# Kernel tuning notes

Measured on AMD Instinct MI355X. Metric: run time of the kernel, lower is better.

The kernel has to match this reference:

```python
import jax, jax.numpy as jnp
import numpy as np

N = 8192
K = 64
EPS = 1e-7
BN_EPS = 1e-5


def _norm(x):
    return jnp.sqrt(jnp.sum(x * x, axis=-1, keepdims=True))


def _bn(x, gamma, beta):
    # BatchNorm2d in training mode (batch statistics, biased variance)
    mu = jnp.mean(x, axis=(0, 2, 3), keepdims=True)
    var = jnp.mean((x - mu) ** 2, axis=(0, 2, 3), keepdims=True)
    return gamma.reshape(1, -1, 1, 1) * (x - mu) / jnp.sqrt(var + BN_EPS) + beta.reshape(1, -1, 1, 1)


def _conv1x1(x, w, b):
    # 1x1 conv == per-pixel linear: x [B,C,H,W], w [O,C]
    return jnp.einsum('bchw,oc->bohw', x, w) + b.reshape(1, -1, 1, 1)


def setup_inputs() -> dict:
    key = jax.random.key(0)
    ks = jax.random.split(key, 24)
    d = {}
    d['points'] = jax.random.normal(ks[0], (1, N, 3), jnp.float32)
    # graph_conv weights (torch code re-draws these every forward; here fixed params)
    lim0 = float(np.sqrt(6.0 / (4 + 64)))
    d['gw0'] = jax.random.uniform(ks[1], (4, 64), jnp.float32, -lim0, lim0)
    lim = float(np.sqrt(6.0 / (64 + 64)))
    for i in range(1, 5):
        d[f'gw{i}'] = jax.random.uniform(ks[1 + i], (64, 64), jnp.float32, -lim, lim)
    # mlp_1: 4->64->128, mlp_2: 192->256->1024 (1x1 convs + BN)
    d['c1w'] = jax.random.normal(ks[6], (64, 4), jnp.float32) * 0.1
    d['c1b'] = jnp.zeros((64,), jnp.float32)
    d['bn1g'] = jnp.ones((64,), jnp.float32)
    d['bn1b'] = jnp.zeros((64,), jnp.float32)
    d['c2w'] = jax.random.normal(ks[7], (128, 64), jnp.float32) * 0.1
    d['c2b'] = jnp.zeros((128,), jnp.float32)
    d['bn2g'] = jnp.ones((128,), jnp.float32)
    d['bn2b'] = jnp.zeros((128,), jnp.float32)
    d['c3w'] = jax.random.normal(ks[8], (256, 192), jnp.float32) * 0.05
    d['c3b'] = jnp.zeros((256,), jnp.float32)
    d['bn3g'] = jnp.ones((256,), jnp.float32)
    d['bn3b'] = jnp.zeros((256,), jnp.float32)
    d['c4w'] = jax.random.normal(ks[9], (1024, 256), jnp.float32) * 0.05
    d['c4b'] = jnp.zeros((1024,), jnp.float32)
    d['bn4g'] = jnp.ones((1024,), jnp.float32)
    d['bn4b'] = jnp.zeros((1024,), jnp.float32)
    return d


def _knn_search(points, k):
    # pairwise squared distances via ||a||^2 - 2ab + ||b||^2
    r = jnp.sum(points * points, axis=-1, keepdims=True)          # [1,N,1]
    dis = r - 2.0 * jnp.einsum('bnd,bmd->bnm', points, points) + jnp.swapaxes(r, 1, 2)
    _, idx = jax.lax.top_k(-dis, k)                                # [1,N,K]
    knn_pts = jax.vmap(lambda p, i: p[i])(points, idx)             # [1,N,K,3]
    return knn_pts


def _proj_knn(knn_pts):
    b, n, k, _ = knn_pts.shape
    pc = knn_pts - knn_pts[:, :, :1, :]                            # center on first neighbor (self)
    vn = jnp.sqrt(jnp.sum(pc * pc, axis=-1))                       # [1,N,K]
    id1 = jnp.argmax(vn, axis=-1)                                  # farthest neighbor
    a1 = jnp.take_along_axis(pc, jnp.broadcast_to(id1[:, :, None, None], (b, n, 1, 3)), axis=2)[:, :, 0, :]
    a1 = a1 / (_norm(a1) + EPS)
    a2 = jnp.mean(pc, axis=2)
    a2 = a2 / (_norm(a2) + EPS)
    a3 = a1 + 1.5 * a2
    a3 = a3 / (_norm(a3) + EPS)
    den = _norm(pc) + EPS                                          # [1,N,K,1]
    f1 = jnp.sum(pc * a1[:, :, None, :], axis=-1, keepdims=True) / den
    f2 = jnp.sum(pc * a2[:, :, None, :], axis=-1, keepdims=True) / den
    f3 = jnp.sum(pc * a3[:, :, None, :], axis=-1, keepdims=True) / den
    return jnp.concatenate([f1, f2, f3, vn[..., None]], axis=-1)   # [1,N,K,4]


def _proj_points(points):
    b, n, _ = points.shape
    vn = jnp.sqrt(jnp.sum(points * points, axis=-1))               # [1,N]
    i1 = jnp.argmax(vn, axis=-1)
    i2 = jnp.argmin(vn, axis=-1)
    a1 = jnp.take_along_axis(points, jnp.broadcast_to(i1[:, None, None], (b, 1, 3)), axis=1)[:, 0, :]
    a1 = a1 / (_norm(a1) + EPS)
    a2 = jnp.take_along_axis(points, jnp.broadcast_to(i2[:, None, None], (b, 1, 3)), axis=1)[:, 0, :]
    a2 = a2 / (_norm(a2) + EPS)
    a3 = a1 + 1.5 * a2
    a3 = a3 / (_norm(a3) + EPS)
    den = _norm(points) + EPS                                      # [1,N,1]
    f1 = jnp.sum(points * a1[:, None, :], axis=-1, keepdims=True) / den
    f2 = jnp.sum(points * a2[:, None, :], axis=-1, keepdims=True) / den
    f3 = jnp.sum(points * a3[:, None, :], axis=-1, keepdims=True) / den
    return jnp.concatenate([f1, f2, f3, vn[..., None]], axis=-1)   # [1,N,4]


def reference(points, gw0, gw1, gw2, gw3, gw4,
              c1w, c1b, bn1g, bn1b, c2w, c2b, bn2g, bn2b,
              c3w, c3b, bn3g, bn3b, c4w, c4b, bn4g, bn4b):
    n = points.shape[1]
    # upper branch: KNN -> rotation-invariant local feats -> 5-layer MLP -> max over K
    knn_pts = _knn_search(points, K)
    feat_up = _proj_knn(knn_pts)                                   # [1,N,K,4]
    x = feat_up.reshape(-1, 4)
    for w in (gw0, gw1, gw2, gw3, gw4):
        x = jax.nn.relu(x @ w)
    x = x.reshape(1, n, K, 64)
    emb_up = jnp.max(x, axis=2, keepdims=True)                     # [1,N,1,64]
    emb_up = emb_up.reshape(1, 64, n, 1)                           # raw view (reshape), as in torch
    # lower branch: global rotation-invariant feats -> mlp_1
    feat_down = _proj_points(points)                               # [1,N,4]
    emb_down = feat_down.reshape(1, 4, n, 1)                       # raw view (reshape), as in torch
    h = jax.nn.relu(_bn(_conv1x1(emb_down, c1w, c1b), bn1g, bn1b))
    h = jax.nn.relu(_bn(_conv1x1(h, c2w, c2b), bn2g, bn2b))        # [1,128,N,1]
    emb = jnp.concatenate([emb_up, h], axis=1)                     # [1,192,N,1]
    out = jax.nn.relu(_bn(_conv1x1(emb, c3w, c3b), bn3g, bn3b))
    out = jax.nn.relu(_bn(_conv1x1(out, c4w, c4b), bn4g, bn4b))    # [1,1024,N,1]
    return out
```

## Files before the change

### kernel.cpp

```cpp
#include <hip/hip_runtime.h>
#include <hip/hip_bf16.h>

#define NPTS 8192
#define KNN 64
#define EPSF 1e-7f

#define OFF_P4      0
#define OFF_STATS   32768
#define OFF_PART    36012
#define OFF_FEATDN  36864
#define OFF_WT1     69632
#define OFF_GWT     69888
#define OFF_BW2     79104
#define OFF_BW3     83200
#define OFF_BW4     107776
#define OFF_XB3V    238848
#define OFF_Y1      2336000
#define OFF_Y2      2860288
#define OFF_Y3      3908864
#define OFF_FEATUP  6006016

typedef __bf16 bf16x8 __attribute__((ext_vector_type(8)));
typedef float  f32x4  __attribute__((ext_vector_type(4)));

__device__ __forceinline__ unsigned f2u(float f) {
    unsigned u = __float_as_uint(f);
    return ((int)u >= 0) ? (u | 0x80000000u) : ~u;
}
__device__ __forceinline__ float key_to_f(unsigned long long k) {
    unsigned v = (unsigned)(k >> 32);
    unsigned ob = (v & 0x80000000u) ? (v ^ 0x80000000u) : ~v;
    return __uint_as_float(ob);
}
__device__ __forceinline__ unsigned short f2bf(float x) {
    union { __bf16 h; unsigned short s; } u;
    u.h = (__bf16)x;
    return u.s;
}
__device__ __forceinline__ unsigned packbf2(float lo, float hi) {
    return (unsigned)f2bf(lo) | ((unsigned)f2bf(hi) << 16);
}
__device__ __forceinline__ unsigned long long u64min(unsigned long long a, unsigned long long b){ return a < b ? a : b; }
__device__ __forceinline__ unsigned long long u64max(unsigned long long a, unsigned long long b){ return a < b ? b : a; }

__device__ __forceinline__ unsigned long long sort_merge(
    unsigned long long key, unsigned long long cur, int lane)
{
    #pragma unroll
    for (int k = 2; k <= 64; k <<= 1) {
        #pragma unroll
        for (int j = k >> 1; j > 0; j >>= 1) {
            unsigned long long o = __shfl_xor(key, j);
            bool up = ((lane & k) == 0);
            bool lower = ((lane & j) == 0);
            key = (lower == up) ? u64min(key, o) : u64max(key, o);
        }
    }
    unsigned long long rev = __shfl(key, 63 - lane);
    unsigned long long m = u64min(cur, rev);
    #pragma unroll
    for (int j = 32; j > 0; j >>= 1) {
        unsigned long long o = __shfl_xor(m, j);
        m = ((lane & j) == 0) ? u64min(m, o) : u64max(m, o);
    }
    return m;
}

__global__ __launch_bounds__(256) void prepwt_kernel(
    const float* __restrict__ points,
    const float* __restrict__ c1w, const float* __restrict__ c2w,
    const float* __restrict__ c3w, const float* __restrict__ c4w,
    const float* __restrict__ gw0, const float* __restrict__ gw1,
    const float* __restrict__ gw2, const float* __restrict__ gw3,
    const float* __restrict__ gw4,
    float* __restrict__ ws)
{
    const int t = blockIdx.x * 256 + threadIdx.x;
    const int T = 256 * 256;
    for (int m = t; m < 2944; m += T) ws[OFF_STATS + m] = 0.f;
    for (int m = t; m < 64*4; m += T) { int o = m >> 2, c = m & 3; ws[OFF_WT1 + c*64 + o] = c1w[m]; }

    unsigned short* bw2 = (unsigned short*)(ws + OFF_BW2);
    for (int m = t; m < 128*64; m += T)   bw2[m] = f2bf(c2w[m]);
    unsigned short* bw3 = (unsigned short*)(ws + OFF_BW3);
    for (int m = t; m < 256*192; m += T)  bw3[m] = f2bf(c3w[m]);
    unsigned short* bw4 = (unsigned short*)(ws + OFF_BW4);
    for (int m = t; m < 1024*256; m += T) bw4[m] = f2bf(c4w[m]);

    unsigned short* gwt = (unsigned short*)(ws + OFF_GWT);
    for (int m = t; m < 2048; m += T) {
        int o = m >> 5, i = m & 31;
        gwt[m] = (i < 4) ? f2bf(gw0[i*64 + o]) : (unsigned short)0;
    }
    const float* gsrc[4] = {gw1, gw2, gw3, gw4};
    for (int l = 0; l < 4; ++l) {
        const float* g = gsrc[l];
        unsigned short* dst = gwt + 2048 + l*4096;
        for (int m = t; m < 4096; m += T) { int o = m >> 6, i = m & 63; dst[m] = f2bf(g[i*64 + o]); }
    }

    if (blockIdx.x < 32) {
        const int n = blockIdx.x * 256 + threadIdx.x;
        float x = points[3*n+0], y = points[3*n+1], z = points[3*n+2];
        float rr = x*x + y*y + z*z;
        ((float4*)(ws + OFF_P4))[n] = make_float4(x, y, z, rr);
        float vn = sqrtf(rr);
        unsigned b = __float_as_uint(vn);
        unsigned long long mxk = ((unsigned long long)b << 32) | (unsigned long long)(0xFFFFFFFFu - (unsigned)n);
        unsigned long long mnk = ((unsigned long long)b << 32) | (unsigned long long)(unsigned)n;
        for (int j = 32; j > 0; j >>= 1) {
            mxk = u64max(mxk, __shfl_xor(mxk, j));
            mnk = u64min(mnk, __shfl_xor(mnk, j));
        }
        __shared__ unsigned long long smx[4], smn[4];
        int wid = threadIdx.x >> 6;
        if ((threadIdx.x & 63) == 0) { smx[wid] = mxk; smn[wid] = mnk; }
        __syncthreads();
        if (threadIdx.x == 0) {
            unsigned long long MX = 0ull, MN = ~0ull;
            for (int i = 0; i < 4; ++i) { MX = u64max(MX, smx[i]); MN = u64min(MN, smn[i]); }
            unsigned long long* parts = (unsigned long long*)(ws + OFF_PART);
            parts[2*blockIdx.x + 0] = MX;
            parts[2*blockIdx.x + 1] = MN;
        }
    }
}

__global__ __launch_bounds__(512) void knn_feat_kernel(
    const float4* __restrict__ p4, float4* __restrict__ feat_up,
    float* __restrict__ ws)
{
    __shared__ __align__(16) float4 scand[2048];
    __shared__ unsigned long long queue[8][128];
    const int lane = threadIdx.x & 63;
    const int wid  = threadIdx.x >> 6;
    const int q = blockIdx.x * 8 + wid;

    const float4 qa = p4[q];
    unsigned long long cur = ~0ull;
    float ke = __builtin_inff();
    int qc = 0;
    unsigned long long* Q = queue[wid];

    for (int base = 0; base < NPTS; base += 2048) {
        __syncthreads();
        for (int t = threadIdx.x; t < 2048; t += 512) scand[t] = p4[base + t];
        __syncthreads();
        #pragma unroll 2
        for (int sub = 0; sub < 2048; sub += 128) {
            float4 cd0 = scand[sub + lane];
            float4 cd1 = scand[sub + 64 + lane];
            float dot0 = fmaf(qa.x, cd0.x, fmaf(qa.y, cd0.y, qa.z * cd0.z));
            float dot1 = fmaf(qa.x, cd1.x, fmaf(qa.y, cd1.y, qa.z * cd1.z));
            float e0 = fmaf(-2.f, dot0, cd0.w);
            float e1 = fmaf(-2.f, dot1, cd1.w);
            bool p0 = e0 < ke;
            bool p1 = e1 < ke;
            unsigned long long m0 = __ballot(p0);
            unsigned long long m1 = __ballot(p1);
            if (m0) {
                int prefix = __builtin_amdgcn_mbcnt_hi((unsigned)(m0 >> 32),
                              __builtin_amdgcn_mbcnt_lo((unsigned)m0, 0));
                if (p0) Q[qc + prefix] = ((unsigned long long)f2u(e0) << 32)
                                       | (unsigned long long)(unsigned)(base + sub + lane);
                qc += __popcll(m0);
                if (qc >= 64) {
                    qc -= 64;
                    cur = sort_merge(Q[qc + lane], cur, lane);
                    ke = key_to_f(__shfl(cur, 63));
                }
            }
            if (m1) {
                int prefix = __builtin_amdgcn_mbcnt_hi((unsigned)(m1 >> 32),
                              __builtin_amdgcn_mbcnt_lo((unsigned)m1, 0));
                if (p1) Q[qc + prefix] = ((unsigned long long)f2u(e1) << 32)
                                       | (unsigned long long)(unsigned)(base + sub + 64 + lane);
                qc += __popcll(m1);
                if (qc >= 64) {
                    qc -= 64;
                    cur = sort_merge(Q[qc + lane], cur, lane);
                    ke = key_to_f(__shfl(cur, 63));
                }
            }
        }
    }
    cur = sort_merge((lane < qc) ? Q[lane] : ~0ull, cur, lane);

    int nidx = (int)(unsigned)(cur & 0xFFFFFFFFu);
    float4 np = p4[nidx];
    float ox = __shfl(np.x, 0), oy = __shfl(np.y, 0), oz = __shfl(np.z, 0);
    float pcx = np.x - ox, pcy = np.y - oy, pcz = np.z - oz;
    float vn = sqrtf(pcx*pcx + pcy*pcy + pcz*pcz);

    unsigned long long ak = ((unsigned long long)__float_as_uint(vn) << 32)
                          | (unsigned long long)(unsigned)(63 - lane);
    for (int s = 32; s > 0; s >>= 1) ak = u64max(ak, __shfl_xor(ak, s));
    int id1 = 63 - (int)(unsigned)(ak & 0xFFFFFFFFu);

    float a1x = __shfl(pcx, id1), a1y = __shfl(pcy, id1), a1z = __shfl(pcz, id1);
    float n1 = sqrtf(a1x*a1x + a1y*a1y + a1z*a1z) + EPSF;
    a1x /= n1; a1y /= n1; a1z /= n1;

    float sx = pcx, sy = pcy, sz = pcz;
    for (int s = 32; s > 0; s >>= 1) {
        sx += __shfl_xor(sx, s); sy += __shfl_xor(sy, s); sz += __shfl_xor(sz, s);
    }
    float a2x = sx * (1.f/64.f), a2y = sy * (1.f/64.f), a2z = sz * (1.f/64.f);
    float n2 = sqrtf(a2x*a2x + a2y*a2y + a2z*a2z) + EPSF;
    a2x /= n2; a2y /= n2; a2z /= n2;

    float a3x = a1x + 1.5f*a2x, a3y = a1y + 1.5f*a2y, a3z = a1z + 1.5f*a2z;
    float n3 = sqrtf(a3x*a3x + a3y*a3y + a3z*a3z) + EPSF;
    a3x /= n3; a3y /= n3; a3z /= n3;

    float den = vn + EPSF;
    float f1 = (pcx*a1x + pcy*a1y + pcz*a1z) / den;
    float f2 = (pcx*a2x + pcy*a2y + pcz*a2z) / den;
    float f3 = (pcx*a3x + pcy*a3y + pcz*a3z) / den;
    feat_up[q*64 + lane] = make_float4(f1, f2, f3, vn);

    {
        const unsigned long long* parts = (const unsigned long long*)(ws + OFF_PART);
        unsigned long long mxk = (lane < 32) ? parts[2*lane + 0] : 0ull;
        unsigned long long mnk = (lane < 32) ? parts[2*lane + 1] : ~0ull;
        for (int s = 32; s > 0; s >>= 1) {
            mxk = u64max(mxk, __shfl_xor(mxk, s));
            mnk = u64min(mnk, __shfl_xor(mnk, s));
        }
        if (lane == 0) {
            int i1 = (int)(0xFFFFFFFFu - (unsigned)(mxk & 0xFFFFFFFFu));
            int i2 = (int)(unsigned)(mnk & 0xFFFFFFFFu);
            float4 p1 = p4[i1];
            float4 p2 = p4[i2];
            float w1 = sqrtf(p1.x*p1.x + p1.y*p1.y + p1.z*p1.z) + EPSF;
            float b1x = p1.x/w1, b1y = p1.y/w1, b1z = p1.z/w1;
            float w2 = sqrtf(p2.x*p2.x + p2.y*p2.y + p2.z*p2.z) + EPSF;
            float b2x = p2.x/w2, b2y = p2.y/w2, b2z = p2.z/w2;
            float b3x = b1x + 1.5f*b2x, b3y = b1y + 1.5f*b2y, b3z = b1z + 1.5f*b2z;
            float w3 = sqrtf(b3x*b3x + b3y*b3y + b3z*b3z) + EPSF;
            b3x /= w3; b3y /= w3; b3z /= w3;
            float vq = sqrtf(qa.w);
            float dq = vq + EPSF;
            float g1 = (qa.x*b1x + qa.y*b1y + qa.z*b1z) / dq;
            float g2 = (qa.x*b2x + qa.y*b2y + qa.z*b2z) / dq;
            float g3 = (qa.x*b3x + qa.y*b3y + qa.z*b3z) / dq;
            ((float4*)(ws + OFF_FEATDN))[q] = make_float4(g1, g2, g3, vq);
        }
    }
}

#define BROW 72
__global__ __launch_bounds__(256) void mlp_kernel(
    const float4* __restrict__ feat_up,
    const unsigned short* __restrict__ gwt,
    unsigned short* __restrict__ xb3v)
{
    __shared__ __align__(16) unsigned short Blds[4][64 * BROW];
    const int lane = threadIdx.x & 63;
    const int wid  = threadIdx.x >> 6;
    const int q = blockIdx.x * 4 + wid;
    const int c = lane & 15, g = lane >> 4;
    unsigned short* B = Blds[wid];

    {
        float4 f = feat_up[q*64 + lane];
        uint2 p0;
        p0.x = packbf2(f.x, f.y);
        p0.y = packbf2(f.z, f.w);
        *(uint2*)&B[lane*BROW] = p0;
        *(uint2*)&B[lane*BROW + 4] = make_uint2(0, 0);
        uint4 z4 = make_uint4(0, 0, 0, 0);
        *(uint4*)&B[lane*BROW + 8]  = z4;
        *(uint4*)&B[lane*BROW + 16] = z4;
        *(uint4*)&B[lane*BROW + 24] = z4;
    }

    const unsigned short* Wl[5] = {gwt, gwt + 2048, gwt + 6144, gwt + 10240, gwt + 14336};
    f32x4 acc[4][4];

    for (int layer = 0; layer < 5; ++layer) {
        const int wstride = (layer == 0) ? 32 : 64;
        const int nks = (layer == 0) ? 1 : 2;
        #pragma unroll
        for (int mb = 0; mb < 4; ++mb)
            #pragma unroll
            for (int nb = 0; nb < 4; ++nb)
                acc[mb][nb] = (f32x4){0.f, 0.f, 0.f, 0.f};

        for (int ks = 0; ks < nks; ++ks) {
            bf16x8 af[4], bf[4];
            #pragma unroll
            for (int mb = 0; mb < 4; ++mb)
                af[mb] = *(const bf16x8*)(Wl[layer] + (mb*16 + c)*wstride + ks*32 + g*8);
            #pragma unroll
            for (int nb = 0; nb < 4; ++nb)
                bf[nb] = *(const bf16x8*)&B[(nb*16 + c)*BROW + ks*32 + g*8];
            #pragma unroll
            for (int mb = 0; mb < 4; ++mb)
                #pragma unroll
                for (int nb = 0; nb < 4; ++nb)
                    acc[mb][nb] = __builtin_amdgcn_mfma_f32_16x16x32_bf16(af[mb], bf[nb], acc[mb][nb], 0, 0, 0);
        }

        if (layer < 4) {
            #pragma unroll
            for (int mb = 0; mb < 4; ++mb) {
                #pragma unroll
                for (int nb = 0; nb < 4; ++nb) {
                    f32x4 a = acc[mb][nb];
                    uint2 pw;
                    pw.x = packbf2(fmaxf(a[0], 0.f), fmaxf(a[1], 0.f));
                    pw.y = packbf2(fmaxf(a[2], 0.f), fmaxf(a[3], 0.f));
                    *(uint2*)&B[(nb*16 + c)*BROW + mb*16 + g*4] = pw;
                }
            }
        }
    }

    const int cc = q >> 7;
    const int pbase = (q & 127) << 6;
    #pragma unroll
    for (int mb = 0; mb < 4; ++mb) {
        float v[4];
        #pragma unroll
        for (int r = 0; r < 4; ++r)
            v[r] = fmaxf(fmaxf(fmaxf(acc[mb][0][r], acc[mb][1][r]),
                               fmaxf(acc[mb][2][r], acc[mb][3][r])), 0.f);
        #pragma unroll
        for (int mask = 1; mask <= 8; mask <<= 1)
            #pragma unroll
            for (int r = 0; r < 4; ++r)
                v[r] = fmaxf(v[r], __shfl_xor(v[r], mask));
        if (c == 0) {
            #pragma unroll
            for (int r = 0; r < 4; ++r) {
                const int f = mb*16 + g*4 + r;
                xb3v[(size_t)(pbase + f) * 64 + cc] = f2bf(v[r]);
            }
        }
    }
}

__global__ __launch_bounds__(256) void conv1_kernel(
    const float* __restrict__ x, const float* __restrict__ wt,
    const float* __restrict__ bias, float* __restrict__ y,
    float* __restrict__ stout)
{
    const int tid = threadIdx.x;
    const int p  = blockIdx.x * 256 + tid;
    const int o0 = blockIdx.y * 32;
    float acc[32];
    #pragma unroll
    for (int u = 0; u < 32; ++u) acc[u] = bias[o0 + u];
    #pragma unroll
    for (int c = 0; c < 4; ++c) {
        float xv = x[c * NPTS + p];
        const float* wr = wt + c * 64 + o0;
        #pragma unroll
        for (int u = 0; u < 32; ++u) acc[u] = fmaf(xv, wr[u], acc[u]);
    }
    #pragma unroll
    for (int u = 0; u < 32; ++u) y[(o0 + u) * NPTS + p] = acc[u];

    __shared__ float ps[4][32], pss[4][32];
    const int wid = tid >> 6, lane = tid & 63;
    #pragma unroll
    for (int u = 0; u < 32; ++u) {
        float s = acc[u], ss = acc[u] * acc[u];
        for (int j = 32; j > 0; j >>= 1) { s += __shfl_xor(s, j); ss += __shfl_xor(ss, j); }
        if (lane == 0) { ps[wid][u] = s; pss[wid][u] = ss; }
    }
    __syncthreads();
    if (tid < 32) {
        float S  = ps[0][tid] + ps[1][tid] + ps[2][tid] + ps[3][tid];
        float SS = pss[0][tid] + pss[1][tid] + pss[2][tid] + pss[3][tid];
        atomicAdd(&stout[o0 + tid], S);
        atomicAdd(&stout[64 + o0 + tid], SS);
    }
}

__global__ __launch_bounds__(256) void convbn_kernel(
    const unsigned short* __restrict__ A,
    const unsigned short* __restrict__ Bdir, int Kdir,
    const float* __restrict__ yprev,
    const float* __restrict__ stp, const float* __restrict__ gam, const float* __restrict__ bet,
    const float* __restrict__ bias, int K, int M,
    float* __restrict__ yout, float* __restrict__ stout)
{
    __shared__ float sc[256], sh[256];
    const int tid = threadIdx.x;
    const int Cp = K - Kdir;
    for (int cc = tid; cc < Cp; cc += 256) {
        float mu  = stp[cc] * (1.f / 8192.f);
        float var = stp[Cp + cc] * (1.f / 8192.f) - mu * mu;
        float s = gam[cc] / sqrtf(var + 1e-5f);
        sc[cc] = s; sh[cc] = bet[cc] - mu * s;
    }
    __syncthreads();

    const int lane = tid & 63;
    const int w = tid >> 6;
    const int n0 = blockIdx.x * 256 + w * 64;
    const int m0 = blockIdx.y * 64;
    const int c = lane & 15, g = lane >> 4;

    f32x4 acc[4][4];
    #pragma unroll
    for (int mt = 0; mt < 4; ++mt)
        #pragma unroll
        for (int nt = 0; nt < 4; ++nt)
            acc[mt][nt] = (f32x4){0.f, 0.f, 0.f, 0.f};

    for (int k0 = 0; k0 < K; k0 += 32) {
        bf16x8 af[4], bf[4];
        #pragma unroll
        for (int mt = 0; mt < 4; ++mt)
            af[mt] = *(const bf16x8*)(A + (size_t)(m0 + mt*16 + c) * K + k0 + g*8);
        if (k0 + 32 <= Kdir) {
            #pragma unroll
            for (int nt = 0; nt < 4; ++nt)
                bf[nt] = *(const bf16x8*)(Bdir + (size_t)(n0 + nt*16 + c) * Kdir + k0 + g*8);
        } else {
            const int ch0 = k0 - Kdir + g*8;
            #pragma unroll
            for (int nt = 0; nt < 4; ++nt) {
                const int pt = n0 + nt*16 + c;
                bf16x8 r;
                #pragma unroll
                for (int j = 0; j < 8; ++j) {
                    float vv = fmaxf(fmaf(yprev[(size_t)(ch0 + j) * NPTS + pt],
                                          sc[ch0 + j], sh[ch0 + j]), 0.f);
                    r[j] = (__bf16)vv;
                }
                bf[nt] = r;
            }
        }
        #pragma unroll
        for (int mt = 0; mt < 4; ++mt)
            #pragma unroll
            for (int nt = 0; nt < 4; ++nt)
                acc[mt][nt] = __builtin_amdgcn_mfma_f32_16x16x32_bf16(af[mt], bf[nt], acc[mt][nt], 0, 0, 0);
    }

    #pragma unroll
    for (int mt = 0; mt < 4; ++mt) {
        float s[4], ss[4];
        #pragma unroll
        for (int r = 0; r < 4; ++r) {
            const int o = m0 + mt*16 + g*4 + r;
            const float bv = bias[o];
            float sum = 0.f, sq = 0.f;
            #pragma unroll
            for (int nt = 0; nt < 4; ++nt) {
                float v = acc[mt][nt][r] + bv;
                yout[(size_t)o * NPTS + n0 + nt*16 + c] = v;
                sum += v; sq += v * v;
            }
            s[r] = sum; ss[r] = sq;
        }
        #pragma unroll
        for (int mask = 1; mask <= 8; mask <<= 1)
            #pragma unroll
            for (int r = 0; r < 4; ++r) {
                s[r]  += __shfl_xor(s[r],  mask);
                ss[r] += __shfl_xor(ss[r], mask);
            }
        if (c == 0) {
            #pragma unroll
            for (int r = 0; r < 4; ++r) {
                const int o = m0 + mt*16 + g*4 + r;
                atomicAdd(&stout[o], s[r]);
                atomicAdd(&stout[M + o], ss[r]);
            }
        }
    }
}

__global__ __launch_bounds__(256) void bnrelu_kernel(
    const float4* y, const float* __restrict__ st,
    const float* __restrict__ g, const float* __restrict__ b,
    float4* out, int C)
{
    int idx = blockIdx.x * 256 + threadIdx.x;
    int c = idx >> 11;
    float mu  = st[c] * (1.f / 8192.f);
    float var = st[C + c] * (1.f / 8192.f) - mu * mu;
    float scale = g[c] / sqrtf(var + 1e-5f);
    float sh = b[c] - mu * scale;
    float4 v = y[idx];
    v.x = fmaxf(fmaf(v.x, scale, sh), 0.f);
    v.y = fmaxf(fmaf(v.y, scale, sh), 0.f);
    v.z = fmaxf(fmaf(v.z, scale, sh), 0.f);
    v.w = fmaxf(fmaf(v.w, scale, sh), 0.f);
    out[idx] = v;
}

extern "C" void kernel_launch(void* const* d_in, const int* in_sizes, int n_in,
                              void* d_out, int out_size, void* d_ws, size_t ws_size,
                              hipStream_t stream) {
    const float* points = (const float*)d_in[0];
    const float* gw0 = (const float*)d_in[1];
    const float* gw1 = (const float*)d_in[2];
    const float* gw2 = (const float*)d_in[3];
    const float* gw3 = (const float*)d_in[4];
    const float* gw4 = (const float*)d_in[5];
    const float* c1w = (const float*)d_in[6];  const float* c1b = (const float*)d_in[7];
    const float* bn1g = (const float*)d_in[8]; const float* bn1b = (const float*)d_in[9];
    const float* c2w = (const float*)d_in[10]; const float* c2b = (const float*)d_in[11];
    const float* bn2g = (const float*)d_in[12];const float* bn2b = (const float*)d_in[13];
    const float* c3w = (const float*)d_in[14]; const float* c3b = (const float*)d_in[15];
    const float* bn3g = (const float*)d_in[16];const float* bn3b = (const float*)d_in[17];
    const float* c4w = (const float*)d_in[18]; const float* c4b = (const float*)d_in[19];
    const float* bn4g = (const float*)d_in[20];const float* bn4b = (const float*)d_in[21];

    float* ws = (float*)d_ws;
    float* p4f    = ws + OFF_P4;
    float* featdn = ws + OFF_FEATDN;
    float* featup = ws + OFF_FEATUP;
    float* y1 = ws + OFF_Y1; float* y2 = ws + OFF_Y2; float* y3 = ws + OFF_Y3;
    float* s1 = ws + OFF_STATS + 0;
    float* s2 = ws + OFF_STATS + 128;
    float* s3 = ws + OFF_STATS + 384;
    float* s4 = ws + OFF_STATS + 896;
    float* wt1 = ws + OFF_WT1;
    const unsigned short* gwt = (const unsigned short*)(ws + OFF_GWT);
    const unsigned short* bw2 = (const unsigned short*)(ws + OFF_BW2);
    const unsigned short* bw3 = (const unsigned short*)(ws + OFF_BW3);
    const unsigned short* bw4 = (const unsigned short*)(ws + OFF_BW4);
    unsigned short* xb3v = (unsigned short*)(ws + OFF_XB3V);
    float* outp = (float*)d_out;

    prepwt_kernel<<<256, 256, 0, stream>>>(points, c1w, c2w, c3w, c4w,
                                           gw0, gw1, gw2, gw3, gw4, ws);

    knn_feat_kernel<<<1024, 512, 0, stream>>>((const float4*)p4f, (float4*)featup, ws);
    mlp_kernel<<<2048, 256, 0, stream>>>((const float4*)featup, gwt, xb3v);

    conv1_kernel<<<dim3(32, 2), 256, 0, stream>>>(featdn, wt1, c1b, y1, s1);
    convbn_kernel<<<dim3(32, 2), 256, 0, stream>>>(bw2, nullptr, 0, y1, s1, bn1g, bn1b,
                                                   c2b, 64, 128, y2, s2);
    convbn_kernel<<<dim3(32, 4), 256, 0, stream>>>(bw3, xb3v, 64, y2, s2, bn2g, bn2b,
                                                   c3b, 192, 256, y3, s3);
    convbn_kernel<<<dim3(32, 16), 256, 0, stream>>>(bw4, nullptr, 0, y3, s3, bn3g, bn3b,
                                                    c4b, 256, 1024, outp, s4);
    bnrelu_kernel<<<8192, 256, 0, stream>>>((const float4*)outp, s4, bn4g, bn4b, (float4*)outp, 1024);
}
```

Before: 331.1 us.

## Fold conv1 stats into mlp kernel and recompute conv1 inside conv2

```diff
diff --git a/kernel.cpp b/kernel.cpp
--- a/kernel.cpp
+++ b/kernel.cpp
@@ -15,7 +15,6 @@
 #define OFF_BW3     83200
 #define OFF_BW4     107776
 #define OFF_XB3V    238848
-#define OFF_Y1      2336000
 #define OFF_Y2      2860288
 #define OFF_Y3      3908864
 #define OFF_FEATUP  6006016
@@ -253,7 +252,9 @@
 __global__ __launch_bounds__(256) void mlp_kernel(
     const float4* __restrict__ feat_up,
     const unsigned short* __restrict__ gwt,
-    unsigned short* __restrict__ xb3v)
+    unsigned short* __restrict__ xb3v,
+    const float* __restrict__ c1b,
+    float* __restrict__ ws)
 {
     __shared__ __align__(16) unsigned short Blds[4][64 * BROW];
     const int lane = threadIdx.x & 63;
@@ -339,43 +340,143 @@
             }
         }
     }
-}
-
-__global__ __launch_bounds__(256) void conv1_kernel(
-    const float* __restrict__ x, const float* __restrict__ wt,
-    const float* __restrict__ bias, float* __restrict__ y,
-    float* __restrict__ stout)
+
+    if (blockIdx.x < 64) {
+        __syncthreads();
+        float* sps  = (float*)&Blds[0][0];
+        float* spss = sps + 128;
+        const int tid = threadIdx.x;
+        const int bx = blockIdx.x & 31, by = blockIdx.x >> 5;
+        const int p  = bx * 256 + tid;
+        const int o0 = by * 32;
+        const float* fdn = ws + OFF_FEATDN;
+        const float* wt1 = ws + OFF_WT1;
+        float* s1 = ws + OFF_STATS;
+        float xv0 = fdn[p], xv1 = fdn[8192 + p], xv2 = fdn[16384 + p], xv3 = fdn[24576 + p];
+        float accc[32];
+        #pragma unroll
+        for (int u = 0; u < 32; ++u) accc[u] = c1b[o0 + u];
+        #pragma unroll
+        for (int u = 0; u < 32; ++u) accc[u] = fmaf(xv0, wt1[0*64 + o0 + u], accc[u]);
+        #pragma unroll
+        for (int u = 0; u < 32; ++u) accc[u] = fmaf(xv1, wt1[1*64 + o0 + u], accc[u]);
+        #pragma unroll
+        for (int u = 0; u < 32; ++u) accc[u] = fmaf(xv2, wt1[2*64 + o0 + u], accc[u]);
+        #pragma unroll
+        for (int u = 0; u < 32; ++u) accc[u] = fmaf(xv3, wt1[3*64 + o0 + u], accc[u]);
+        #pragma unroll
+        for (int u = 0; u < 32; ++u) {
+            float s = accc[u], ss = accc[u] * accc[u];
+            for (int j = 32; j > 0; j >>= 1) { s += __shfl_xor(s, j); ss += __shfl_xor(ss, j); }
+            if (lane == 0) { sps[wid*32 + u] = s; spss[wid*32 + u] = ss; }
+        }
+        __syncthreads();
+        if (tid < 32) {
+            float S  = sps[tid] + sps[32 + tid] + sps[64 + tid] + sps[96 + tid];
+            float SS = spss[tid] + spss[32 + tid] + spss[64 + tid] + spss[96 + tid];
+            atomicAdd(&s1[o0 + tid], S);
+            atomicAdd(&s1[64 + o0 + tid], SS);
+        }
+    }
+}
+
+__global__ __launch_bounds__(256) void conv2fd_kernel(
+    const unsigned short* __restrict__ A,
+    const float* __restrict__ c1b,
+    const float* __restrict__ stp, const float* __restrict__ gam, const float* __restrict__ bet,
+    const float* __restrict__ bias, float* __restrict__ yout, float* __restrict__ stout,
+    const float* __restrict__ ws)
 {
+    __shared__ float sc[64], sh[64], swt[256], sb[64];
     const int tid = threadIdx.x;
-    const int p  = blockIdx.x * 256 + tid;
-    const int o0 = blockIdx.y * 32;
-    float acc[32];
+    if (tid < 64) {
+        float mu  = stp[tid] * (1.f / 8192.f);
+        float var = stp[64 + tid] * (1.f / 8192.f) - mu * mu;
+        float s = gam[tid] / sqrtf(var + 1e-5f);
+        sc[tid] = s; sh[tid] = bet[tid] - mu * s;
+        sb[tid] = c1b[tid];
+    }
+    if (tid < 256) swt[tid] = ws[OFF_WT1 + tid];
+    __syncthreads();
+
+    const float* fdn = ws + OFF_FEATDN;
+    const int lane = tid & 63;
+    const int w = tid >> 6;
+    const int n0 = blockIdx.x * 256 + w * 64;
+    const int m0 = blockIdx.y * 64;
+    const int c = lane & 15, g = lane >> 4;
+    const int K = 64, M = 128;
+
+    f32x4 acc[4][4];
     #pragma unroll
-    for (int u = 0; u < 32; ++u) acc[u] = bias[o0 + u];
+    for (int mt = 0; mt < 4; ++mt)
+        #pragma unroll
+        for (int nt = 0; nt < 4; ++nt)
+            acc[mt][nt] = (f32x4){0.f, 0.f, 0.f, 0.f};
+
+    for (int k0 = 0; k0 < K; k0 += 32) {
+        bf16x8 af[4], bf[4];
+        #pragma unroll
+        for (int mt = 0; mt < 4; ++mt)
+            af[mt] = *(const bf16x8*)(A + (size_t)(m0 + mt*16 + c) * K + k0 + g*8);
+        const int ch0 = k0 + g*8;
+        #pragma unroll
+        for (int nt = 0; nt < 4; ++nt) {
+            const int pt = n0 + nt*16 + c;
+            const float fd0 = fdn[pt];
+            const float fd1 = fdn[8192 + pt];
+            const float fd2 = fdn[16384 + pt];
+            const float fd3 = fdn[24576 + pt];
+            bf16x8 r;
+            #pragma unroll
+            for (int j = 0; j < 8; ++j) {
+                const int ch = ch0 + j;
+                float v = fmaf(fd3, swt[192 + ch],
+                          fmaf(fd2, swt[128 + ch],
+                          fmaf(fd1, swt[64 + ch],
+                          fmaf(fd0, swt[ch], sb[ch]))));
+                r[j] = (__bf16)fmaxf(fmaf(v, sc[ch], sh[ch]), 0.f);
+            }
+            bf[nt] = r;
+        }
+        #pragma unroll
+        for (int mt = 0; mt < 4; ++mt)
+            #pragma unroll
+            for (int nt = 0; nt < 4; ++nt)
+                acc[mt][nt] = __builtin_amdgcn_mfma_f32_16x16x32_bf16(af[mt], bf[nt], acc[mt][nt], 0, 0, 0);
+    }
+
     #pragma unroll
-    for (int c = 0; c < 4; ++c) {
-        float xv = x[c * NPTS + p];
-        const float* wr = wt + c * 64 + o0;
-        #pragma unroll
-        for (int u = 0; u < 32; ++u) acc[u] = fmaf(xv, wr[u], acc[u]);
-    }
-    #pragma unroll
-    for (int u = 0; u < 32; ++u) y[(o0 + u) * NPTS + p] = acc[u];
-
-    __shared__ float ps[4][32], pss[4][32];
-    const int wid = tid >> 6, lane = tid & 63;
-    #pragma unroll
-    for (int u = 0; u < 32; ++u) {
-        float s = acc[u], ss = acc[u] * acc[u];
-        for (int j = 32; j > 0; j >>= 1) { s += __shfl_xor(s, j); ss += __shfl_xor(ss, j); }
-        if (lane == 0) { ps[wid][u] = s; pss[wid][u] = ss; }
-    }
-    __syncthreads();
-    if (tid < 32) {
-        float S  = ps[0][tid] + ps[1][tid] + ps[2][tid] + ps[3][tid];
-        float SS = pss[0][tid] + pss[1][tid] + pss[2][tid] + pss[3][tid];
-        atomicAdd(&stout[o0 + tid], S);
-        atomicAdd(&stout[64 + o0 + tid], SS);
+    for (int mt = 0; mt < 4; ++mt) {
+        float s[4], ss[4];
+        #pragma unroll
+        for (int r = 0; r < 4; ++r) {
+            const int o = m0 + mt*16 + g*4 + r;
+            const float bv = bias[o];
+            float sum = 0.f, sq = 0.f;
+            #pragma unroll
+            for (int nt = 0; nt < 4; ++nt) {
+                float v = acc[mt][nt][r] + bv;
+                yout[(size_t)o * NPTS + n0 + nt*16 + c] = v;
+                sum += v; sq += v * v;
+            }
+            s[r] = sum; ss[r] = sq;
+        }
+        #pragma unroll
+        for (int mask = 1; mask <= 8; mask <<= 1)
+            #pragma unroll
+            for (int r = 0; r < 4; ++r) {
+                s[r]  += __shfl_xor(s[r],  mask);
+                ss[r] += __shfl_xor(ss[r], mask);
+            }
+        if (c == 0) {
+            #pragma unroll
+            for (int r = 0; r < 4; ++r) {
+                const int o = m0 + mt*16 + g*4 + r;
+                atomicAdd(&stout[o], s[r]);
+                atomicAdd(&stout[M + o], ss[r]);
+            }
+        }
     }
 }
 
@@ -515,14 +616,12 @@
 
     float* ws = (float*)d_ws;
     float* p4f    = ws + OFF_P4;
-    float* featdn = ws + OFF_FEATDN;
     float* featup = ws + OFF_FEATUP;
-    float* y1 = ws + OFF_Y1; float* y2 = ws + OFF_Y2; float* y3 = ws + OFF_Y3;
+    float* y2 = ws + OFF_Y2; float* y3 = ws + OFF_Y3;
     float* s1 = ws + OFF_STATS + 0;
     float* s2 = ws + OFF_STATS + 128;
     float* s3 = ws + OFF_STATS + 384;
     float* s4 = ws + OFF_STATS + 896;
-    float* wt1 = ws + OFF_WT1;
     const unsigned short* gwt = (const unsigned short*)(ws + OFF_GWT);
     const unsigned short* bw2 = (const unsigned short*)(ws + OFF_BW2);
     const unsigned short* bw3 = (const unsigned short*)(ws + OFF_BW3);
@@ -534,11 +633,10 @@
                                            gw0, gw1, gw2, gw3, gw4, ws);
 
     knn_feat_kernel<<<1024, 512, 0, stream>>>((const float4*)p4f, (float4*)featup, ws);
-    mlp_kernel<<<2048, 256, 0, stream>>>((const float4*)featup, gwt, xb3v);
-
-    conv1_kernel<<<dim3(32, 2), 256, 0, stream>>>(featdn, wt1, c1b, y1, s1);
-    convbn_kernel<<<dim3(32, 2), 256, 0, stream>>>(bw2, nullptr, 0, y1, s1, bn1g, bn1b,
-                                                   c2b, 64, 128, y2, s2);
+    mlp_kernel<<<2048, 256, 0, stream>>>((const float4*)featup, gwt, xb3v, c1b, ws);
+
+    conv2fd_kernel<<<dim3(32, 2), 256, 0, stream>>>(bw2, c1b, s1, bn1g, bn1b,
+                                                    c2b, y2, s2, ws);
     convbn_kernel<<<dim3(32, 4), 256, 0, stream>>>(bw3, xb3v, 64, y2, s2, bn2g, bn2b,
                                                    c3b, 192, 256, y3, s3);
     convbn_kernel<<<dim3(32, 16), 256, 0, stream>>>(bw4, nullptr, 0, y3, s3, bn3g, bn3b,
```

After: 325.4 us (median of 2 runs). Within noise of the previous version (-1.7%).
